# Optimization experiments

Measured on AMD Instinct MI355X. Metric: run time of the kernel, lower is better.

The kernel has to match this reference:

```python
import jax, jax.numpy as jnp
import numpy as np

DIM = 512
H = 8
D = 64
EPS = 1e-5


def _ln(x, g, b):
    m = jnp.mean(x, axis=-1, keepdims=True)
    v = jnp.var(x, axis=-1, keepdims=True)
    return (x - m) * jax.lax.rsqrt(v + EPS) * g + b


def _attn(x, ctx, wq, wk, wv, wo, bo):
    B, S, _ = x.shape
    T = ctx.shape[1]
    q = (x @ wq).reshape(B, S, H, D)
    k = (ctx @ wk).reshape(B, T, H, D)
    v = (ctx @ wv).reshape(B, T, H, D)
    scale = D ** -0.5
    score = jnp.einsum('bqhd,bkhd->bhqk', q, k) * scale  # [B,H,S,T]
    w = jax.nn.softmax(score, axis=-1)
    o = jnp.einsum('bhqk,bkhd->bqhd', w, v).reshape(B, S, H * D)
    return o @ wo + bo


def _geglu(x, w, b):
    h = x @ w + b
    y, gate = h[..., :4 * DIM], h[..., 4 * DIM:]
    tanh_res = jnp.tanh(gate * 0.7978845608 * (1.0 + 0.044715 * gate * gate))
    return y * 0.5 * gate * (1.0 + tanh_res)


def setup_inputs() -> dict:
    key = jax.random.key(0)
    ks = jax.random.split(key, 16)
    s = 0.02
    inp = {
        'x': jax.random.normal(ks[0], (2, 4096, DIM), jnp.float32),
        'context': jax.random.normal(ks[1], (2, 77, DIM), jnp.float32),
        'ln1_g': jnp.ones((DIM,), jnp.float32),
        'ln1_b': jnp.zeros((DIM,), jnp.float32),
        'wq1': jax.random.normal(ks[2], (DIM, H * D), jnp.float32) * s,
        'wk1': jax.random.normal(ks[3], (DIM, H * D), jnp.float32) * s,
        'wv1': jax.random.normal(ks[4], (DIM, H * D), jnp.float32) * s,
        'wo1': jax.random.normal(ks[5], (H * D, H * D), jnp.float32) * s,
        'bo1': jnp.zeros((H * D,), jnp.float32),
        'ln2_g': jnp.ones((DIM,), jnp.float32),
        'ln2_b': jnp.zeros((DIM,), jnp.float32),
        'wq2': jax.random.normal(ks[6], (DIM, H * D), jnp.float32) * s,
        'wk2': jax.random.normal(ks[7], (DIM, H * D), jnp.float32) * s,
        'wv2': jax.random.normal(ks[8], (DIM, H * D), jnp.float32) * s,
        'wo2': jax.random.normal(ks[9], (H * D, H * D), jnp.float32) * s,
        'bo2': jnp.zeros((H * D,), jnp.float32),
        'ln3_g': jnp.ones((DIM,), jnp.float32),
        'ln3_b': jnp.zeros((DIM,), jnp.float32),
        'geglu_w': jax.random.normal(ks[10], (DIM, 8 * DIM), jnp.float32) * s,
        'geglu_b': jnp.zeros((8 * DIM,), jnp.float32),
        'out_w': jax.random.normal(ks[11], (4 * DIM, DIM), jnp.float32) * s,
        'out_b': jnp.zeros((DIM,), jnp.float32),
    }
    return inp


def reference(x, context, ln1_g, ln1_b, wq1, wk1, wv1, wo1, bo1,
              ln2_g, ln2_b, wq2, wk2, wv2, wo2, bo2,
              ln3_g, ln3_b, geglu_w, geglu_b, out_w, out_b):
    h = _attn(_ln(x, ln1_g, ln1_b), _ln(x, ln1_g, ln1_b), wq1, wk1, wv1, wo1, bo1) + x
    h = _attn(_ln(h, ln2_g, ln2_b), context, wq2, wk2, wv2, wo2, bo2) + h
    ff = _geglu(_ln(h, ln3_g, ln3_b), geglu_w, geglu_b)
    return ff @ out_w + out_b + h
```

## Files before the change

kernel.cpp:

```cpp
#include <hip/hip_runtime.h>
#include <hip/hip_bf16.h>
#include <math.h>

#define DIM 512
#define NHEAD 8
#define HD 64
#define BATCH 2
#define SEQ 4096
#define CTXLEN 77
#define NTOK (BATCH*SEQ)
#define NCTX (BATCH*CTXLEN)

typedef __hip_bfloat16 bf16;
typedef __attribute__((ext_vector_type(8))) short bf8_t;
typedef __attribute__((ext_vector_type(4))) float f4_t;

__device__ __forceinline__ float b2f(bf16 v){ return __bfloat162float(v); }
__device__ __forceinline__ bf16  f2b(float v){ return __float2bfloat16(v); }
__device__ __forceinline__ unsigned short f2bu(float v){ bf16 h = f2b(v); return *(unsigned short*)&h; }
__device__ __forceinline__ unsigned int packbf2(float a, float b){
    unsigned int au = __float_as_uint(a) + 0x8000u;
    unsigned int bu = __float_as_uint(b) + 0x8000u;
    return __builtin_amdgcn_perm(bu, au, 0x07060302u);
}
__device__ __forceinline__ void  stf(float* p, float v){ *p = v; }
__device__ __forceinline__ void  stf(bf16* p, float v){ *p = f2b(v); }

__global__ __launch_bounds__(256)
void ln_kernel(const float* __restrict__ x, const float* __restrict__ g,
               const float* __restrict__ b, bf16* __restrict__ out, int nrows)
{
    int row  = blockIdx.x * 4 + (threadIdx.x >> 6);
    int lane = threadIdx.x & 63;
    if (row >= nrows) return;
    const float* xr = x + (size_t)row * DIM;
    float v[8];
    float s = 0.f, sq = 0.f;
    #pragma unroll
    for (int j = 0; j < 8; ++j) {
        float f = xr[lane + 64*j];
        v[j] = f; s += f; sq += f*f;
    }
    #pragma unroll
    for (int off = 32; off; off >>= 1) {
        s  += __shfl_xor(s,  off);
        sq += __shfl_xor(sq, off);
    }
    float mean = s * (1.f/DIM);
    float var  = sq * (1.f/DIM) - mean*mean;
    float rstd = rsqrtf(var + 1e-5f);
    bf16* orow = out + (size_t)row * DIM;
    #pragma unroll
    for (int j = 0; j < 8; ++j) {
        int c = lane + 64*j;
        orow[c] = f2b((v[j]-mean)*rstd*g[c] + b[c]);
    }
}

__global__ __launch_bounds__(256)
void transpose_bf16_kernel(const float* __restrict__ W, bf16* __restrict__ Wt, int K, int N)
{
    __shared__ float tile[32][33];
    int n0 = blockIdx.x * 32, k0 = blockIdx.y * 32;
    int tx = threadIdx.x & 31, ty = threadIdx.x >> 5;
    #pragma unroll
    for (int p = 0; p < 4; ++p)
        tile[ty + p*8][tx] = W[(size_t)(k0 + ty + p*8)*N + n0 + tx];
    __syncthreads();
    #pragma unroll
    for (int p = 0; p < 4; ++p)
        Wt[(size_t)(n0 + ty + p*8)*K + k0 + tx] = f2b(tile[tx][ty + p*8]);
}

struct TPtrs { const float* src[8]; bf16* dst[8]; };
__global__ __launch_bounds__(256)
void transpose8_kernel(TPtrs p)
{
    __shared__ float tile[32][33];
    const float* W = p.src[blockIdx.z];
    bf16* Wt = p.dst[blockIdx.z];
    int n0 = blockIdx.x * 32, k0 = blockIdx.y * 32;
    int tx = threadIdx.x & 31, ty = threadIdx.x >> 5;
    #pragma unroll
    for (int q = 0; q < 4; ++q)
        tile[ty + q*8][tx] = W[(size_t)(k0 + ty + q*8)*512 + n0 + tx];
    __syncthreads();
    #pragma unroll
    for (int q = 0; q < 4; ++q)
        Wt[(size_t)(n0 + ty + q*8)*512 + k0 + tx] = f2b(tile[tx][ty + q*8]);
}

__global__ __launch_bounds__(256)
void cast_bf16_kernel(const float* __restrict__ in, bf16* __restrict__ out, int n)
{
    int i = blockIdx.x*256 + threadIdx.x;
    if (i < n) out[i] = f2b(in[i]);
}

__global__ __launch_bounds__(256)
void v_transpose_kernel(const bf16* __restrict__ V, bf16* __restrict__ Vt, int T, int pitch)
{
    __shared__ __align__(16) unsigned short tile[64*64];
    const int tid = threadIdx.x;
    const int b = blockIdx.z, h = blockIdx.y;
    const int t0 = blockIdx.x * 64;
    #pragma unroll
    for (int it = 0; it < 2; ++it) {
        int e = tid + it*256;
        int t = e >> 3, c = e & 7;
        int gk = t0 + t;
        bf8_t v = {0,0,0,0,0,0,0,0};
        if (gk < T) v = *(const bf8_t*)(V + ((size_t)(b*T + gk))*DIM + h*HD + c*8);
        *(bf8_t*)&tile[t*64 + c*8] = v;
    }
    __syncthreads();
    #pragma unroll
    for (int it = 0; it < 2; ++it) {
        int e = tid + it*256;
        int d = e & 63, oc = e >> 6;
        unsigned short tmp[8];
        #pragma unroll
        for (int j = 0; j < 8; ++j) tmp[j] = tile[(oc*8 + j)*64 + d];
        *(bf8_t*)(Vt + ((size_t)((b*8 + h)*64 + d))*pitch + t0 + oc*8) = *(bf8_t*)tmp;
    }
}

struct OutPtrs { void* p[3]; };
template<int RESID, typename OUTT, bool GUARD>
__global__ __launch_bounds__(256)
void gemm_mfma_kernel(const bf16* __restrict__ A, const bf16* __restrict__ Wt,
                      const float* __restrict__ bias, const float* __restrict__ resid,
                      OutPtrs outs, int M, int K)
{
    __shared__ __align__(16) unsigned short As[128*64];
    __shared__ __align__(16) unsigned short Bs[64*64];
    const int tid  = threadIdx.x;
    const int wave = tid >> 6, lane = tid & 63;
    const int l16  = lane & 15, quad = lane >> 4;
    const int wm = (wave >> 1) * 64, wn = (wave & 1) * 32;
    const int m0 = blockIdx.y * 128, n0 = blockIdx.x * 64;
    OUTT* outp = (OUTT*)outs.p[n0 >> 9];
    const int lc0 = n0 & 511;
    const int sr = tid >> 3, sc_ = tid & 7;

    f4_t acc[4][2];
    #pragma unroll
    for (int i = 0; i < 4; ++i) { acc[i][0] = f4_t{0,0,0,0}; acc[i][1] = f4_t{0,0,0,0}; }

    bf8_t pa[4], pb[2];
    #pragma unroll
    for (int p = 0; p < 4; ++p) {
        int r = sr + p*32;
        int gr = m0 + r;
        if (GUARD) gr = (gr < M) ? gr : (M-1);
        pa[p] = *(const bf8_t*)(A + (size_t)gr*K + sc_*8);
    }
    #pragma unroll
    for (int p = 0; p < 2; ++p)
        pb[p] = *(const bf8_t*)(Wt + (size_t)(n0 + sr + p*32)*K + sc_*8);

    for (int k0 = 0; k0 < K; k0 += 64) {
        #pragma unroll
        for (int p = 0; p < 4; ++p) {
            int r = sr + p*32;
            *(bf8_t*)&As[r*64 + ((sc_ ^ (r&7))*8)] = pa[p];
        }
        #pragma unroll
        for (int p = 0; p < 2; ++p) {
            int r = sr + p*32;
            *(bf8_t*)&Bs[r*64 + ((sc_ ^ (r&7))*8)] = pb[p];
        }
        __syncthreads();
        if (k0 + 64 < K) {
            #pragma unroll
            for (int p = 0; p < 4; ++p) {
                int r = sr + p*32;
                int gr = m0 + r;
                if (GUARD) gr = (gr < M) ? gr : (M-1);
                pa[p] = *(const bf8_t*)(A + (size_t)gr*K + k0 + 64 + sc_*8);
            }
            #pragma unroll
            for (int p = 0; p < 2; ++p)
                pb[p] = *(const bf8_t*)(Wt + (size_t)(n0 + sr + p*32)*K + k0 + 64 + sc_*8);
        }
        #pragma unroll
        for (int kc = 0; kc < 2; ++kc) {
            const int cg = kc*4 + quad;
            bf8_t af[4], bfr[2];
            #pragma unroll
            for (int mt = 0; mt < 4; ++mt) {
                int r = wm + mt*16 + l16;
                af[mt] = *(const bf8_t*)&As[r*64 + ((cg ^ (r&7))*8)];
            }
            #pragma unroll
            for (int nt = 0; nt < 2; ++nt) {
                int r = wn + nt*16 + l16;
                bfr[nt] = *(const bf8_t*)&Bs[r*64 + ((cg ^ (r&7))*8)];
            }
            #pragma unroll
            for (int mt = 0; mt < 4; ++mt)
                #pragma unroll
                for (int nt = 0; nt < 2; ++nt)
                    acc[mt][nt] = __builtin_amdgcn_mfma_f32_16x16x32_bf16(af[mt], bfr[nt], acc[mt][nt], 0, 0, 0);
        }
        __syncthreads();
    }

    #pragma unroll
    for (int mt = 0; mt < 4; ++mt) {
        #pragma unroll
        for (int r_ = 0; r_ < 4; ++r_) {
            int row = m0 + wm + mt*16 + quad*4 + r_;
            if (GUARD && row >= M) continue;
            size_t rb = (size_t)row * 512;
            #pragma unroll
            for (int nt = 0; nt < 2; ++nt) {
                int col = lc0 + wn + nt*16 + l16;
                float v = acc[mt][nt][r_];
                if (bias) v += bias[col];
                if (RESID) v += resid[rb + col];
                stf(&outp[rb + col], v);
            }
        }
    }
}

__global__ __launch_bounds__(256)
void geglu_mfma_kernel(const bf16* __restrict__ A, const bf16* __restrict__ WtG,
                       const float* __restrict__ bias, bf16* __restrict__ outp)
{
    __shared__ __align__(16) unsigned short As[128*64];
    __shared__ __align__(16) unsigned short Bys[64*64];
    __shared__ __align__(16) unsigned short Bgs[64*64];
    const int tid  = threadIdx.x;
    const int wave = tid >> 6, lane = tid & 63;
    const int l16  = lane & 15, quad = lane >> 4;
    const int m0 = blockIdx.y * 128, n0 = blockIdx.x * 64;
    const int sr = tid >> 3, sc_ = tid & 7;

    f4_t accy[2][4], accg[2][4];
    #pragma unroll
    for (int i = 0; i < 2; ++i)
        #pragma unroll
        for (int j = 0; j < 4; ++j) { accy[i][j] = f4_t{0,0,0,0}; accg[i][j] = f4_t{0,0,0,0}; }

    bf8_t pa[4], py[2], pg[2];
    #pragma unroll
    for (int p = 0; p < 4; ++p)
        pa[p] = *(const bf8_t*)(A + (size_t)(m0 + sr + p*32)*DIM + sc_*8);
    #pragma unroll
    for (int p = 0; p < 2; ++p) {
        py[p] = *(const bf8_t*)(WtG + (size_t)(n0 + sr + p*32)*DIM + sc_*8);
        pg[p] = *(const bf8_t*)(WtG + (size_t)(2048 + n0 + sr + p*32)*DIM + sc_*8);
    }

    for (int k0 = 0; k0 < DIM; k0 += 64) {
        #pragma unroll
        for (int p = 0; p < 4; ++p) {
            int r = sr + p*32;
            *(bf8_t*)&As[r*64 + ((sc_ ^ (r&7))*8)] = pa[p];
        }
        #pragma unroll
        for (int p = 0; p < 2; ++p) {
            int r = sr + p*32;
            *(bf8_t*)&Bys[r*64 + ((sc_ ^ (r&7))*8)] = py[p];
            *(bf8_t*)&Bgs[r*64 + ((sc_ ^ (r&7))*8)] = pg[p];
        }
        __syncthreads();
        if (k0 + 64 < DIM) {
            #pragma unroll
            for (int p = 0; p < 4; ++p)
                pa[p] = *(const bf8_t*)(A + (size_t)(m0 + sr + p*32)*DIM + k0 + 64 + sc_*8);
            #pragma unroll
            for (int p = 0; p < 2; ++p) {
                py[p] = *(const bf8_t*)(WtG + (size_t)(n0 + sr + p*32)*DIM + k0 + 64 + sc_*8);
                pg[p] = *(const bf8_t*)(WtG + (size_t)(2048 + n0 + sr + p*32)*DIM + k0 + 64 + sc_*8);
            }
        }
        #pragma unroll
        for (int kc = 0; kc < 2; ++kc) {
            const int cg = kc*4 + quad;
            bf8_t af[2];
            #pragma unroll
            for (int mt = 0; mt < 2; ++mt) {
                int r = wave*32 + mt*16 + l16;
                af[mt] = *(const bf8_t*)&As[r*64 + ((cg ^ (r&7))*8)];
            }
            #pragma unroll
            for (int nt = 0; nt < 4; ++nt) {
                int r = nt*16 + l16;
                bf8_t by = *(const bf8_t*)&Bys[r*64 + ((cg ^ (r&7))*8)];
                bf8_t bg = *(const bf8_t*)&Bgs[r*64 + ((cg ^ (r&7))*8)];
                #pragma unroll
                for (int mt = 0; mt < 2; ++mt) {
                    accy[mt][nt] = __builtin_amdgcn_mfma_f32_16x16x32_bf16(af[mt], by, accy[mt][nt], 0, 0, 0);
                    accg[mt][nt] = __builtin_amdgcn_mfma_f32_16x16x32_bf16(af[mt], bg, accg[mt][nt], 0, 0, 0);
                }
            }
        }
        __syncthreads();
    }

    #pragma unroll
    for (int mt = 0; mt < 2; ++mt) {
        #pragma unroll
        for (int r_ = 0; r_ < 4; ++r_) {
            int row = m0 + wave*32 + mt*16 + quad*4 + r_;
            size_t rb = (size_t)row * 2048;
            #pragma unroll
            for (int nt = 0; nt < 4; ++nt) {
                int col = n0 + nt*16 + l16;
                float y = accy[mt][nt][r_] + bias[col];
                float g = accg[mt][nt][r_] + bias[2048 + col];
                float t = tanhf(0.7978845608f*g*(1.f + 0.044715f*g*g));
                outp[rb + col] = f2b(y * 0.5f * g * (1.f + t));
            }
        }
    }
}

__global__ __launch_bounds__(512)
void attn_mfma_kernel(const bf16* __restrict__ Qm, const bf16* __restrict__ Km,
                      const bf16* __restrict__ VtG, bf16* __restrict__ Om,
                      int T, int vpitch)
{
    __shared__ __align__(16) unsigned short Ks[64*64];
    __shared__ __align__(16) unsigned short Vts[64*64];
    __shared__ __align__(16) unsigned short Ps[8][16*64];

    const int tid  = threadIdx.x;
    const int wave = tid >> 6, lane = tid & 63;
    const int l16  = lane & 15, quad = lane >> 4;
    const int b = blockIdx.z, h = blockIdx.y;
    const int qblk = blockIdx.x * 128;
    const int sr = tid >> 3, sc_ = tid & 7;

    bf8_t ones;
    #pragma unroll
    for (int j = 0; j < 8; ++j) ((unsigned short*)&ones)[j] = 0x3F80;

    bf8_t qf[2];
    {
        const bf16* qp = Qm + ((size_t)(b*SEQ + qblk + wave*16 + l16))*DIM + h*HD + quad*8;
        #pragma unroll
        for (int kc = 0; kc < 2; ++kc) {
            bf8_t v = *(const bf8_t*)(qp + kc*32);
            unsigned short* u = (unsigned short*)&v;
            unsigned int* w = (unsigned int*)&v;
            #pragma unroll
            for (int j = 0; j < 4; ++j) {
                float f0 = b2f(*(bf16*)&u[2*j])   * 0.1803368801f;
                float f1 = b2f(*(bf16*)&u[2*j+1]) * 0.1803368801f;
                w[j] = packbf2(f0, f1);
            }
            qf[kc] = v;
        }
    }

    f4_t o[4];
    #pragma unroll
    for (int dt = 0; dt < 4; ++dt) o[dt] = f4_t{0,0,0,0};
    f4_t lacc = {0,0,0,0};

    bf8_t kq, vq;
    kq = bf8_t{0,0,0,0,0,0,0,0};
    if (sr < T) kq = *(const bf8_t*)(Km + ((size_t)(b*T + sr))*DIM + h*HD + sc_*8);
    vq = *(const bf8_t*)(VtG + ((size_t)((b*8 + h)*64 + sr))*vpitch + sc_*8);

    const int ntiles = (T + 63) >> 6;
    for (int t0 = 0; t0 < ntiles; ++t0) {
        const int kb = t0 << 6;
        *(bf8_t*)&Ks[sr*64 + ((sc_ ^ (sr&7))*8)]  = kq;
        *(bf8_t*)&Vts[sr*64 + ((sc_ ^ (sr&7))*8)] = vq;
        __syncthreads();
        if (t0 + 1 < ntiles) {
            int kbn = kb + 64;
            int gk = kbn + sr;
            kq = bf8_t{0,0,0,0,0,0,0,0};
            if (gk < T) kq = *(const bf8_t*)(Km + ((size_t)(b*T + gk))*DIM + h*HD + sc_*8);
            vq = *(const bf8_t*)(VtG + ((size_t)((b*8 + h)*64 + sr))*vpitch + kbn + sc_*8);
        }

        bf8_t kf[4][2], vf[4][2];
        #pragma unroll
        for (int t = 0; t < 4; ++t) {
            int r = t*16 + l16;
            #pragma unroll
            for (int kc = 0; kc < 2; ++kc) {
                int cg = kc*4 + quad;
                kf[t][kc] = *(const bf8_t*)&Ks[r*64 + ((cg ^ (r&7))*8)];
                vf[t][kc] = *(const bf8_t*)&Vts[r*64 + ((cg ^ (r&7))*8)];
            }
        }
        const bool tail = (kb + 64 > T);

        f4_t sc[4];
        #pragma unroll
        for (int km = 0; km < 4; ++km) {
            f4_t c = {0,0,0,0};
            c = __builtin_amdgcn_mfma_f32_16x16x32_bf16(kf[km][0], qf[0], c, 0, 0, 0);
            c = __builtin_amdgcn_mfma_f32_16x16x32_bf16(kf[km][1], qf[1], c, 0, 0, 0);
            sc[km] = c;
        }
        if (tail) {
            #pragma unroll
            for (int km = 0; km < 4; ++km)
                #pragma unroll
                for (int r = 0; r < 4; ++r)
                    if (kb + km*16 + quad*4 + r >= T) sc[km][r] = -1e30f;
        }
        #pragma unroll
        for (int km = 0; km < 4; ++km) {
            uint2 w;
            w.x = packbf2(exp2f(sc[km][0]), exp2f(sc[km][1]));
            w.y = packbf2(exp2f(sc[km][2]), exp2f(sc[km][3]));
            int chunk = 2*km + (quad >> 1);
            int a = l16*64 + ((chunk ^ (l16 & 7))*8) + (quad & 1)*4;
            *(uint2*)&Ps[wave][a] = w;
        }
        #pragma unroll
        for (int kc = 0; kc < 2; ++kc) {
            int cg = kc*4 + quad;
            bf8_t pf = *(const bf8_t*)&Ps[wave][l16*64 + ((cg ^ (l16 & 7))*8)];
            lacc = __builtin_amdgcn_mfma_f32_16x16x32_bf16(ones, pf, lacc, 0, 0, 0);
            #pragma unroll
            for (int dt = 0; dt < 4; ++dt)
                o[dt] = __builtin_amdgcn_mfma_f32_16x16x32_bf16(vf[dt][kc], pf, o[dt], 0, 0, 0);
        }
        __syncthreads();
    }

    {
        float inv = 1.f / lacc[0];
        int tok = qblk + wave*16 + l16;
        size_t base = ((size_t)(b*SEQ + tok))*DIM + h*HD;
        #pragma unroll
        for (int dt = 0; dt < 4; ++dt) {
            uint2 w;
            w.x = packbf2(o[dt][0]*inv, o[dt][1]*inv);
            w.y = packbf2(o[dt][2]*inv, o[dt][3]*inv);
            *(uint2*)(Om + base + dt*16 + quad*4) = w;
        }
    }
}

extern "C" void kernel_launch(void* const* d_in, const int* in_sizes, int n_in,
                              void* d_out, int out_size, void* d_ws, size_t ws_size,
                              hipStream_t stream)
{
    (void)in_sizes; (void)n_in; (void)out_size; (void)ws_size;
    const float* x    = (const float*)d_in[0];
    const float* ctx  = (const float*)d_in[1];
    const float* ln1g = (const float*)d_in[2];
    const float* ln1b = (const float*)d_in[3];
    const float* wq1  = (const float*)d_in[4];
    const float* wk1  = (const float*)d_in[5];
    const float* wv1  = (const float*)d_in[6];
    const float* wo1  = (const float*)d_in[7];
    const float* bo1  = (const float*)d_in[8];
    const float* ln2g = (const float*)d_in[9];
    const float* ln2b = (const float*)d_in[10];
    const float* wq2  = (const float*)d_in[11];
    const float* wk2  = (const float*)d_in[12];
    const float* wv2  = (const float*)d_in[13];
    const float* wo2  = (const float*)d_in[14];
    const float* bo2  = (const float*)d_in[15];
    const float* ln3g = (const float*)d_in[16];
    const float* ln3b = (const float*)d_in[17];
    const float* gw   = (const float*)d_in[18];
    const float* gb   = (const float*)d_in[19];
    const float* ow   = (const float*)d_in[20];
    const float* ob   = (const float*)d_in[21];
    float* out = (float*)d_out;

    char* ws = (char*)d_ws;
    bf16* An  = (bf16*)(ws);
    bf16* VtG = (bf16*)(ws);
    bf16* Qb  = (bf16*)(ws + ((size_t)8<<20));
    bf16* Kb  = (bf16*)(ws + ((size_t)16<<20));
    bf16* Vb  = (bf16*)(ws + ((size_t)24<<20));
    bf16* Ob  = (bf16*)(ws + ((size_t)32<<20));
    bf16* FF  = Qb;
    float* Hf = out;
    bf16* WT  = (bf16*)(ws + ((size_t)40<<20));
    bf16* wq1T = WT + 0*262144, *wk1T = WT + 1*262144, *wv1T = WT + 2*262144, *wo1T = WT + 3*262144;
    bf16* wq2T = WT + 4*262144, *wk2T = WT + 5*262144, *wv2T = WT + 6*262144, *wo2T = WT + 7*262144;
    bf16* gwT  = (bf16*)(ws + ((size_t)44<<20));
    bf16* owT  = (bf16*)(ws + ((size_t)48<<20));
    bf16* ctxb = (bf16*)(ws + ((size_t)50<<20));
    bf16* VtG2 = (bf16*)(ws + ((size_t)50<<20) + ((size_t)512<<10));

    dim3 blk(256);
    dim3 blkA(512);

    TPtrs tp;
    tp.src[0]=wq1; tp.src[1]=wk1; tp.src[2]=wv1; tp.src[3]=wo1;
    tp.src[4]=wq2; tp.src[5]=wk2; tp.src[6]=wv2; tp.src[7]=wo2;
    tp.dst[0]=wq1T; tp.dst[1]=wk1T; tp.dst[2]=wv1T; tp.dst[3]=wo1T;
    tp.dst[4]=wq2T; tp.dst[5]=wk2T; tp.dst[6]=wv2T; tp.dst[7]=wo2T;
    transpose8_kernel<<<dim3(16,16,8), blk, 0, stream>>>(tp);
    transpose_bf16_kernel<<<dim3(128,16), blk, 0, stream>>>(gw, gwT, DIM, 4096);
    transpose_bf16_kernel<<<dim3(16,64), blk, 0, stream>>>(ow, owT, 2048, DIM);
    cast_bf16_kernel<<<dim3((NCTX*DIM+255)/256), blk, 0, stream>>>(ctx, ctxb, NCTX*DIM);

    dim3 gLN(NTOK/4);
    dim3 gQKV(24, 64);
    dim3 gG(8, 64);
    dim3 gKVx(16, 2);
    dim3 gGEGLU(32, 64);
    dim3 gATT(SEQ/128, NHEAD, BATCH);
    OutPtrs oQKV{{Qb, Kb, Vb}};
    OutPtrs oKVx{{Kb, Vb, nullptr}};
    OutPtrs oQ{{Qb, nullptr, nullptr}};
    OutPtrs oH{{Hf, nullptr, nullptr}};
    OutPtrs oOut{{out, nullptr, nullptr}};

    ln_kernel<<<gLN, blk, 0, stream>>>(x, ln1g, ln1b, An, NTOK);
    gemm_mfma_kernel<0,bf16,false><<<gQKV, blk, 0, stream>>>(An, wq1T, nullptr, nullptr, oQKV, NTOK, DIM);
    v_transpose_kernel<<<dim3(SEQ/64, NHEAD, BATCH), blk, 0, stream>>>(Vb, VtG, SEQ, SEQ);
    attn_mfma_kernel<<<gATT, blkA, 0, stream>>>(Qb, Kb, VtG, Ob, SEQ, SEQ);
    gemm_mfma_kernel<1,float,false><<<gG, blk, 0, stream>>>(Ob, wo1T, bo1, x, oH, NTOK, DIM);

    ln_kernel<<<gLN, blk, 0, stream>>>(Hf, ln2g, ln2b, An, NTOK);
    gemm_mfma_kernel<0,bf16,false><<<gG, blk, 0, stream>>>(An, wq2T, nullptr, nullptr, oQ, NTOK, DIM);
    gemm_mfma_kernel<0,bf16,true><<<gKVx, blk, 0, stream>>>(ctxb, wk2T, nullptr, nullptr, oKVx, NCTX, DIM);
    v_transpose_kernel<<<dim3(2, NHEAD, BATCH), blk, 0, stream>>>(Vb, VtG2, CTXLEN, 128);
    attn_mfma_kernel<<<gATT, blkA, 0, stream>>>(Qb, Kb, VtG2, Ob, CTXLEN, 128);
    gemm_mfma_kernel<1,float,false><<<gG, blk, 0, stream>>>(Ob, wo2T, bo2, Hf, oH, NTOK, DIM);

    ln_kernel<<<gLN, blk, 0, stream>>>(Hf, ln3g, ln3b, An, NTOK);
    geglu_mfma_kernel<<<gGEGLU, blk, 0, stream>>>(An, gwT, gb, FF);
    gemm_mfma_kernel<1,float,false><<<gG, blk, 0, stream>>>(FF, owT, ob, Hf, oOut, NTOK, 2048);
}
```

Before: 470.4 us.

## Double-buffer K/V tiles and pass softmax probabilities via lane permutes

The attention kernel now double-buffers the K and V^T tiles in shared memory, so each iteration needs one barrier instead of two and the next tile's store overlaps with the current compute. It also drops the per-wave LDS round trip for the probability tile and rebuilds the MFMA B-operand in registers using permlane32/permlane16 swaps. This cuts LDS traffic and barriers at the cost of twice the K/V shared memory, and it depends on the permlane swap builtins being available on this target and lining up with the MFMA operand layout.

New measurement: 468.1 us. No clear change (-0.5%).

```diff
diff --git a/kernel.cpp b/kernel.cpp
--- a/kernel.cpp
+++ b/kernel.cpp
@@ -324,9 +324,8 @@
                       const bf16* __restrict__ VtG, bf16* __restrict__ Om,
                       int T, int vpitch)
 {
-    __shared__ __align__(16) unsigned short Ks[64*64];
-    __shared__ __align__(16) unsigned short Vts[64*64];
-    __shared__ __align__(16) unsigned short Ps[8][16*64];
+    __shared__ __align__(16) unsigned short Ks[2][64*64];
+    __shared__ __align__(16) unsigned short Vts[2][64*64];
 
     const int tid  = threadIdx.x;
     const int wave = tid >> 6, lane = tid & 63;
@@ -366,19 +365,20 @@
     kq = bf8_t{0,0,0,0,0,0,0,0};
     if (sr < T) kq = *(const bf8_t*)(Km + ((size_t)(b*T + sr))*DIM + h*HD + sc_*8);
     vq = *(const bf8_t*)(VtG + ((size_t)((b*8 + h)*64 + sr))*vpitch + sc_*8);
+    *(bf8_t*)&Ks[0][sr*64 + ((sc_ ^ (sr&7))*8)]  = kq;
+    *(bf8_t*)&Vts[0][sr*64 + ((sc_ ^ (sr&7))*8)] = vq;
+    __syncthreads();
 
     const int ntiles = (T + 63) >> 6;
     for (int t0 = 0; t0 < ntiles; ++t0) {
         const int kb = t0 << 6;
-        *(bf8_t*)&Ks[sr*64 + ((sc_ ^ (sr&7))*8)]  = kq;
-        *(bf8_t*)&Vts[sr*64 + ((sc_ ^ (sr&7))*8)] = vq;
-        __syncthreads();
-        if (t0 + 1 < ntiles) {
-            int kbn = kb + 64;
-            int gk = kbn + sr;
+        const int cur = t0 & 1;
+        const bool havenext = (t0 + 1 < ntiles);
+        if (havenext) {
+            int gk = kb + 64 + sr;
             kq = bf8_t{0,0,0,0,0,0,0,0};
             if (gk < T) kq = *(const bf8_t*)(Km + ((size_t)(b*T + gk))*DIM + h*HD + sc_*8);
-            vq = *(const bf8_t*)(VtG + ((size_t)((b*8 + h)*64 + sr))*vpitch + kbn + sc_*8);
+            vq = *(const bf8_t*)(VtG + ((size_t)((b*8 + h)*64 + sr))*vpitch + kb + 64 + sc_*8);
         }
 
         bf8_t kf[4][2], vf[4][2];
@@ -388,46 +388,52 @@
             #pragma unroll
             for (int kc = 0; kc < 2; ++kc) {
                 int cg = kc*4 + quad;
-                kf[t][kc] = *(const bf8_t*)&Ks[r*64 + ((cg ^ (r&7))*8)];
-                vf[t][kc] = *(const bf8_t*)&Vts[r*64 + ((cg ^ (r&7))*8)];
+                kf[t][kc] = *(const bf8_t*)&Ks[cur][r*64 + ((cg ^ (r&7))*8)];
+                vf[t][kc] = *(const bf8_t*)&Vts[cur][r*64 + ((cg ^ (r&7))*8)];
             }
         }
         const bool tail = (kb + 64 > T);
 
-        f4_t sc[4];
+        f4_t sc4[4];
         #pragma unroll
         for (int km = 0; km < 4; ++km) {
             f4_t c = {0,0,0,0};
             c = __builtin_amdgcn_mfma_f32_16x16x32_bf16(kf[km][0], qf[0], c, 0, 0, 0);
             c = __builtin_amdgcn_mfma_f32_16x16x32_bf16(kf[km][1], qf[1], c, 0, 0, 0);
-            sc[km] = c;
+            sc4[km] = c;
         }
         if (tail) {
             #pragma unroll
             for (int km = 0; km < 4; ++km)
                 #pragma unroll
                 for (int r = 0; r < 4; ++r)
-                    if (kb + km*16 + quad*4 + r >= T) sc[km][r] = -1e30f;
-        }
+                    if (kb + km*16 + quad*4 + r >= T) sc4[km][r] = -1e30f;
+        }
+        unsigned int pk[4][2];
         #pragma unroll
         for (int km = 0; km < 4; ++km) {
-            uint2 w;
-            w.x = packbf2(exp2f(sc[km][0]), exp2f(sc[km][1]));
-            w.y = packbf2(exp2f(sc[km][2]), exp2f(sc[km][3]));
-            int chunk = 2*km + (quad >> 1);
-            int a = l16*64 + ((chunk ^ (l16 & 7))*8) + (quad & 1)*4;
-            *(uint2*)&Ps[wave][a] = w;
+            pk[km][0] = packbf2(exp2f(sc4[km][0]), exp2f(sc4[km][1]));
+            pk[km][1] = packbf2(exp2f(sc4[km][2]), exp2f(sc4[km][3]));
         }
         #pragma unroll
         for (int kc = 0; kc < 2; ++kc) {
-            int cg = kc*4 + quad;
-            bf8_t pf = *(const bf8_t*)&Ps[wave][l16*64 + ((cg ^ (l16 & 7))*8)];
+            auto s0 = __builtin_amdgcn_permlane32_swap(pk[2*kc][0], pk[2*kc+1][0], false, false);
+            auto w02 = __builtin_amdgcn_permlane16_swap(s0[0], s0[1], false, false);
+            auto s1 = __builtin_amdgcn_permlane32_swap(pk[2*kc][1], pk[2*kc+1][1], false, false);
+            auto w13 = __builtin_amdgcn_permlane16_swap(s1[0], s1[1], false, false);
+            union { unsigned int u[4]; bf8_t v; } pfu;
+            pfu.u[0] = w02[0]; pfu.u[1] = w13[0]; pfu.u[2] = w02[1]; pfu.u[3] = w13[1];
+            bf8_t pf = pfu.v;
             lacc = __builtin_amdgcn_mfma_f32_16x16x32_bf16(ones, pf, lacc, 0, 0, 0);
             #pragma unroll
             for (int dt = 0; dt < 4; ++dt)
                 o[dt] = __builtin_amdgcn_mfma_f32_16x16x32_bf16(vf[dt][kc], pf, o[dt], 0, 0, 0);
         }
-        __syncthreads();
+        if (havenext) {
+            *(bf8_t*)&Ks[cur^1][sr*64 + ((sc_ ^ (sr&7))*8)]  = kq;
+            *(bf8_t*)&Vts[cur^1][sr*64 + ((sc_ ^ (sr&7))*8)] = vq;
+            __syncthreads();
+        }
     }
 
     {
```
